# Kernel tuning notes

Measured on AMD Instinct MI355X. Metric: run time of the kernel, lower is better.

The kernel has to match this reference:

```python
import jax, jax.numpy as jnp
import numpy as np

N_HEAD = 12


def setup_inputs() -> dict:
    key = jax.random.key(0)
    ks = jax.random.split(key, 16)
    B, N, D, P, H = 1, 512, 384, 128, N_HEAD
    s = 0.02
    return {
        'x1d': jax.random.normal(ks[0], (B, N, D), jnp.float32),
        'x2d': jax.random.normal(ks[1], (B, N, N, P), jnp.float32),
        'pose_t': jax.random.normal(ks[2], (B, N, 3), jnp.float32),
        'pose_r': jax.random.normal(ks[3], (B, N, 3, 3), jnp.float32),
        'bias': jnp.zeros((B, 1, N, N), jnp.float32),
        'w_sq': jax.random.normal(ks[4], (D, D), jnp.float32) * s,
        'w_sk': jax.random.normal(ks[5], (D, D), jnp.float32) * s,
        'w_sv': jax.random.normal(ks[6], (D, D), jnp.float32) * s,
        'w_pb': jax.random.normal(ks[7], (P, H), jnp.float32) * s,
        'w_pq': jax.random.normal(ks[8], (D, H * 3 * 4), jnp.float32) * s,
        'w_pk': jax.random.normal(ks[9], (D, H * 3 * 4), jnp.float32) * s,
        'w_pv': jax.random.normal(ks[10], (D, H * 3 * 8), jnp.float32) * s,
        'tpw': jax.random.uniform(ks[11], (H,), jnp.float32),
        'w_pairv': jax.random.normal(ks[12], (P, D), jnp.float32) * s,
        'w_out': jax.random.normal(ks[13], (2 * D + H * 8 * 4, D), jnp.float32) * s,
        'b_out': jnp.zeros((D,), jnp.float32),
    }


def reference(x1d, x2d, pose_t, pose_r, bias, w_sq, w_sk, w_sv, w_pb,
              w_pq, w_pk, w_pv, tpw, w_pairv, w_out, b_out):
    B, N, D = x1d.shape
    H = N_HEAD
    dk = D // H
    scalar_w = 1.0 / np.sqrt(3 * dk)
    point_w_c = 1.0 / np.sqrt(3 * 4 * 9 / 2)
    pair_w = 1.0 / np.sqrt(3)

    T = pose_t                                # [B,N,3]
    R = jnp.swapaxes(pose_r, -1, -2)          # [B,N,3,3] (pose[1]^T as in torch code)

    # scalar attention
    q_s = (x1d @ w_sq).reshape(B, N, H, dk)
    k_s = (x1d @ w_sk).reshape(B, N, H, dk)
    v_s = (x1d @ w_sv).reshape(B, N, H, dk)
    scalar_attn = jnp.einsum('bihc,bjhc->bhij', q_s * scalar_w, k_s)

    # point attention (global frame)
    def affine(pt):  # R @ pt + T
        return jnp.einsum('bnxy,bnhpy->bnhpx', R, pt) + T[:, :, None, None, :]

    q_p = affine((x1d @ w_pq).reshape(B, N, H, 4, 3))
    k_p = affine((x1d @ w_pk).reshape(B, N, H, 4, 3))
    v_p = affine((x1d @ w_pv).reshape(B, N, H, 8, 3))

    dist = jnp.linalg.norm(q_p[:, :, None] - k_p[:, None], axis=-1)  # [B,I,J,H,P]
    pw = point_w_c * jax.nn.softplus(tpw)                            # [H]
    point_attn = -0.5 * pw[:, None, None] * jnp.transpose(dist.sum(-1), (0, 3, 1, 2))

    # pair bias attention
    pair_attn = pair_w * jnp.transpose(x2d @ w_pb, (0, 3, 1, 2))     # [B,H,I,J]

    attn = jax.nn.softmax(scalar_attn + point_attn + pair_attn + bias, axis=-1)

    # aggregations
    out_scalar = jnp.einsum('bhij,bjhc->bihc', attn, v_s).reshape(B, N, D)

    out_pg = jnp.einsum('bhij,bjhcp->bihcp', attn, v_p)              # [B,I,H,8,3]
    # inverse affine: R^T @ (x - T)
    out_pl = jnp.einsum('bnyx,bnhpy->bnhpx', R, out_pg - T[:, :, None, None, :])
    out_pn = jnp.linalg.norm(out_pl, axis=-1).reshape(B, N, H * 8)
    out_pl = out_pl.reshape(B, N, H * 8 * 3)

    v_pair = (x2d @ w_pairv).reshape(B, N, N, H, dk)
    out_pair = jnp.einsum('bhij,bijhc->bihc', attn, v_pair).reshape(B, N, D)

    feat = jnp.concatenate([out_scalar, out_pl, out_pair, out_pn], axis=-1)
    return feat @ w_out + b_out
```

## Files before the change

kernel.cpp:

```cpp
#include <hip/hip_runtime.h>
#include <hip/hip_bf16.h>
#include <math.h>

#define N_  512
#define D_  384
#define H_  12
#define DK_ 32
#define P_  128

typedef short short8 __attribute__((ext_vector_type(8)));
typedef float f32x4  __attribute__((ext_vector_type(4)));

static __device__ __forceinline__ unsigned short f2bf(float f) {
    union { float f; unsigned int u; } v; v.f = f;
    unsigned int r = (v.u + 0x7FFFu + ((v.u >> 16) & 1u)) >> 16;
    return (unsigned short)r;
}
static __device__ __forceinline__ float bf2f(unsigned short u) {
    union { unsigned int u; float f; } v; v.u = ((unsigned int)u) << 16;
    return v.f;
}
static __device__ __forceinline__ short2 pk2bf(float a, float b) {
    __hip_bfloat162 h = __float22bfloat162_rn(make_float2(a, b));
    return *(short2*)&h;
}
typedef union { short8 v; short2 h2[4]; } s8u;

__global__ __launch_bounds__(384) void k_front(
    const float* __restrict__ x2d, const float* __restrict__ w_pb,
    float* __restrict__ pairlog,
    const float* __restrict__ x1d, const float* __restrict__ pose_t,
    const float* __restrict__ pose_r,
    const float* __restrict__ w_sq, const float* __restrict__ w_sk,
    const float* __restrict__ w_sv, const float* __restrict__ w_pq,
    const float* __restrict__ w_pk, const float* __restrict__ w_pv,
    float* __restrict__ qs, float* __restrict__ kst,
    float* __restrict__ qp, float* __restrict__ kpt,
    unsigned short* __restrict__ vcatT)
{
    __shared__ float raw[8][288];
    __shared__ float Rsh[8][9];
    __shared__ float Tsh[8][3];

    const int t = threadIdx.x;

    if (blockIdx.x < 2048) {
        if (t >= 256) return;
        const int wid  = t >> 6;
        const int lane = t & 63;
        const int quad = lane >> 4;
        const int col  = lane & 15;
        const float pair_w = 0.57735027f;

        short8 bfr[4];
        #pragma unroll
        for (int kt = 0; kt < 4; ++kt) {
            #pragma unroll
            for (int jj = 0; jj < 8; ++jj) {
                int p = kt * 32 + quad * 8 + jj;
                bfr[kt][jj] = (col < 12) ? (short)f2bf(w_pb[p * 12 + col]) : (short)0;
            }
        }
        #pragma unroll
        for (int s = 0; s < 2; ++s) {
            const int T  = blockIdx.x * 8 + wid * 2 + s;
            const int i  = T >> 5;
            const int j0 = (T & 31) << 4;
            const float* xrow = x2d + ((size_t)(i * N_) + j0 + col) * P_;

            f32x4 acc = {0.f, 0.f, 0.f, 0.f};
            #pragma unroll
            for (int kt = 0; kt < 4; ++kt) {
                const int k0 = kt * 32 + quad * 8;
                float4 f0 = *(const float4*)(xrow + k0);
                float4 f1 = *(const float4*)(xrow + k0 + 4);
                s8u afr;
                afr.h2[0] = pk2bf(f0.x, f0.y);
                afr.h2[1] = pk2bf(f0.z, f0.w);
                afr.h2[2] = pk2bf(f1.x, f1.y);
                afr.h2[3] = pk2bf(f1.z, f1.w);
                acc = __builtin_amdgcn_mfma_f32_16x16x32_bf16(afr.v, bfr[kt], acc, 0, 0, 0);
            }
            if (col < 12) {
                #pragma unroll
                for (int r = 0; r < 4; ++r) {
                    int j = j0 + quad * 4 + r;
                    pairlog[((size_t)(col * N_ + i)) * N_ + j] = pair_w * acc[r];
                }
            }
        }
        return;
    }

    const int b   = blockIdx.x - 2048;
    const int seg = b >> 6;
    const int i0  = (b & 63) * 8;

    if (seg < 3) {
        const float* __restrict__ w = (seg == 0) ? w_sq : (seg == 1) ? w_sk : w_sv;
        float acc[8];
        #pragma unroll
        for (int r = 0; r < 8; ++r) acc[r] = 0.f;
        for (int d = 0; d < D_; d += 4) {
            float4 xr[8];
            #pragma unroll
            for (int r = 0; r < 8; ++r)
                xr[r] = *(const float4*)(x1d + (i0 + r) * D_ + d);
            #pragma unroll
            for (int e = 0; e < 4; ++e) {
                float wv = w[(d + e) * D_ + t];
                #pragma unroll
                for (int r = 0; r < 8; ++r)
                    acc[r] += ((const float*)&xr[r])[e] * wv;
            }
        }
        if (seg == 0) {
            #pragma unroll
            for (int r = 0; r < 8; ++r) qs[(i0 + r) * D_ + t] = acc[r];
        } else if (seg == 1) {
            *(float4*)(kst + t * N_ + i0)     = make_float4(acc[0], acc[1], acc[2], acc[3]);
            *(float4*)(kst + t * N_ + i0 + 4) = make_float4(acc[4], acc[5], acc[6], acc[7]);
        } else {
            int h = t >> 5, c = t & 31;
            s8u sv;
            #pragma unroll
            for (int r = 0; r < 4; ++r) sv.h2[r] = pk2bf(acc[2*r], acc[2*r+1]);
            *(short8*)(vcatT + ((size_t)h * 64 + c) * N_ + i0) = sv.v;
        }
    } else {
        if (t < 72) Rsh[t / 9][t % 9] = pose_r[(i0 + t / 9) * 9 + t % 9];
        else if (t < 96) {
            int r = (t - 72) / 3, c = (t - 72) % 3;
            Tsh[r][c] = pose_t[(i0 + r) * 3 + c];
        }

        if (t < 288) {
            const float* __restrict__ w;
            int col, ldw;
            if (seg == 3) {
                if (t < 144) { w = w_pq; col = t;       ldw = 144; }
                else         { w = w_pk; col = t - 144; ldw = 144; }
            } else         { w = w_pv; col = t;       ldw = 288; }
            float acc[8];
            #pragma unroll
            for (int r = 0; r < 8; ++r) acc[r] = 0.f;
            for (int d = 0; d < D_; d += 4) {
                float4 xr[8];
                #pragma unroll
                for (int r = 0; r < 8; ++r)
                    xr[r] = *(const float4*)(x1d + (i0 + r) * D_ + d);
                #pragma unroll
                for (int e = 0; e < 4; ++e) {
                    float wv = w[(d + e) * ldw + col];
                    #pragma unroll
                    for (int r = 0; r < 8; ++r)
                        acc[r] += ((const float*)&xr[r])[e] * wv;
                }
            }
            #pragma unroll
            for (int r = 0; r < 8; ++r) raw[r][t] = acc[r];
        }
        __syncthreads();

        if (t < 288) {
            const int x3   = t % 3;
            const int base = t - x3;
            if (seg == 3) {
                const int c = (t < 144) ? t : t - 144;
                if (t < 144) {
                    #pragma unroll
                    for (int r = 0; r < 8; ++r) {
                        float g = Rsh[r][0 + x3] * raw[r][base]
                                + Rsh[r][3 + x3] * raw[r][base + 1]
                                + Rsh[r][6 + x3] * raw[r][base + 2] + Tsh[r][x3];
                        qp[(i0 + r) * 144 + c] = g;
                    }
                } else {
                    float g[8];
                    #pragma unroll
                    for (int r = 0; r < 8; ++r)
                        g[r] = Rsh[r][0 + x3] * raw[r][base]
                             + Rsh[r][3 + x3] * raw[r][base + 1]
                             + Rsh[r][6 + x3] * raw[r][base + 2] + Tsh[r][x3];
                    *(float4*)(kpt + c * N_ + i0)     = make_float4(g[0], g[1], g[2], g[3]);
                    *(float4*)(kpt + c * N_ + i0 + 4) = make_float4(g[4], g[5], g[6], g[7]);
                }
            } else {
                int h = t / 24, pc = t % 24;
                float g[8];
                #pragma unroll
                for (int r = 0; r < 8; ++r)
                    g[r] = Rsh[r][0 + x3] * raw[r][base]
                         + Rsh[r][3 + x3] * raw[r][base + 1]
                         + Rsh[r][6 + x3] * raw[r][base + 2] + Tsh[r][x3];
                s8u sv;
                #pragma unroll
                for (int r = 0; r < 4; ++r) sv.h2[r] = pk2bf(g[2*r], g[2*r+1]);
                *(short8*)(vcatT + ((size_t)h * 64 + 32 + pc) * N_ + i0) = sv.v;
            }
        }
    }
}

__global__ __launch_bounds__(256) void k_sp_soft(
    const float* __restrict__ qs, const float* __restrict__ kst,
    const float* __restrict__ qp, const float* __restrict__ kpt,
    const float* __restrict__ bias, const float* __restrict__ tpw,
    const float* __restrict__ pairlog,
    unsigned short* __restrict__ attn_bf)
{
    const int h  = blockIdx.x / 128;
    const int i0 = (blockIdx.x % 128) * 4;
    const int t  = threadIdx.x;
    const int lane = t & 63;
    const int wid  = t >> 6;
    __shared__ float qsh[4][32];
    __shared__ float qph[4][12];
    __shared__ float wredm[4][4];
    __shared__ float wreds[4][4];
    if (t < 128) { int il = t / 32, c = t % 32; qsh[il][c] = qs[(i0+il) * D_ + h*32 + c]; }
    else if (t < 176) { int r = t - 128; int il = r / 12, c = r % 12; qph[il][c] = qp[(i0+il)*144 + h*12 + c]; }
    const float pwh = 0.13608276f * log1pf(expf(tpw[h]));
    const float scalar_w = 0.10206207f;
    __syncthreads();

    float v[4][2];
    for (int jh = 0; jh < 2; ++jh) {
        int j = t + jh * 256;
        float kv[32];
        #pragma unroll
        for (int c = 0; c < 32; ++c) kv[c] = kst[(h*32 + c) * N_ + j];
        float kp[12];
        #pragma unroll
        for (int c = 0; c < 12; ++c) kp[c] = kpt[(h*12 + c) * N_ + j];

        #pragma unroll
        for (int il = 0; il < 4; ++il) {
            float s = 0.f;
            #pragma unroll
            for (int c = 0; c < 32; ++c) s += qsh[il][c] * kv[c];
            float dsum = 0.f;
            #pragma unroll
            for (int p = 0; p < 4; ++p) {
                float dx = qph[il][p*3+0] - kp[p*3+0];
                float dy = qph[il][p*3+1] - kp[p*3+1];
                float dz = qph[il][p*3+2] - kp[p*3+2];
                dsum += sqrtf(dx*dx + dy*dy + dz*dz);
            }
            v[il][jh] = scalar_w * s - 0.5f * pwh * dsum
                      + bias[(i0+il) * N_ + j]
                      + pairlog[((size_t)(h * N_ + (i0+il))) * N_ + j];
        }
    }

    #pragma unroll
    for (int il = 0; il < 4; ++il) {
        float mt = fmaxf(v[il][0], v[il][1]);
        #pragma unroll
        for (int off = 1; off < 64; off <<= 1)
            mt = fmaxf(mt, __shfl_xor(mt, off));
        if (lane == 0) wredm[il][wid] = mt;
    }
    __syncthreads();
    float m[4];
    #pragma unroll
    for (int il = 0; il < 4; ++il)
        m[il] = fmaxf(fmaxf(wredm[il][0], wredm[il][1]),
                      fmaxf(wredm[il][2], wredm[il][3]));

    #pragma unroll
    for (int il = 0; il < 4; ++il) {
        float e0 = __expf(v[il][0] - m[il]);
        float e1 = __expf(v[il][1] - m[il]);
        v[il][0] = e0; v[il][1] = e1;
        float st = e0 + e1;
        #pragma unroll
        for (int off = 1; off < 64; off <<= 1)
            st += __shfl_xor(st, off);
        if (lane == 0) wreds[il][wid] = st;
    }
    __syncthreads();
    #pragma unroll
    for (int il = 0; il < 4; ++il) {
        float inv = 1.0f / (wreds[il][0] + wreds[il][1] + wreds[il][2] + wreds[il][3]);
        size_t base = ((size_t)(h * N_ + i0 + il)) * N_;
        attn_bf[base + t]       = f2bf(v[il][0] * inv);
        attn_bf[base + t + 256] = f2bf(v[il][1] * inv);
    }
}

__global__ __launch_bounds__(256) void k_mid(
    const unsigned short* __restrict__ attn_bf,
    const float* __restrict__ x2d,
    const unsigned short* __restrict__ vcatT,
    float* __restrict__ tmp,
    float* __restrict__ feat, float* __restrict__ outpg)
{
    __shared__ float4 at[3][N_];
    __shared__ float red[4][1536];

    const int t = threadIdx.x;

    if (blockIdx.x < 512) {
        const int i = blockIdx.x;
        for (int idx = t; idx < 12 * N_; idx += 256) {
            int h = idx >> 9, j = idx & 511;
            float a = bf2f(attn_bf[((size_t)(h * N_ + i)) * N_ + j]);
            ((float*)&at[h >> 2][j])[h & 3] = a;
        }
        __syncthreads();

        const int p2 = (t & 63) * 2;
        const int jh = t >> 6;
        float acc[12][2];
        #pragma unroll
        for (int h = 0; h < 12; ++h) { acc[h][0] = 0.f; acc[h][1] = 0.f; }
        const float* xb = x2d + (size_t)i * N_ * P_;

        #pragma unroll 4
        for (int j = jh; j < N_; j += 4) {
            float2 x = *(const float2*)(xb + j * P_ + p2);
            float4 a0 = at[0][j], a1 = at[1][j], a2 = at[2][j];
            acc[0][0]  += a0.x*x.x; acc[0][1]  += a0.x*x.y;
            acc[1][0]  += a0.y*x.x; acc[1][1]  += a0.y*x.y;
            acc[2][0]  += a0.z*x.x; acc[2][1]  += a0.z*x.y;
            acc[3][0]  += a0.w*x.x; acc[3][1]  += a0.w*x.y;
            acc[4][0]  += a1.x*x.x; acc[4][1]  += a1.x*x.y;
            acc[5][0]  += a1.y*x.x; acc[5][1]  += a1.y*x.y;
            acc[6][0]  += a1.z*x.x; acc[6][1]  += a1.z*x.y;
            acc[7][0]  += a1.w*x.x; acc[7][1]  += a1.w*x.y;
            acc[8][0]  += a2.x*x.x; acc[8][1]  += a2.x*x.y;
            acc[9][0]  += a2.y*x.x; acc[9][1]  += a2.y*x.y;
            acc[10][0] += a2.z*x.x; acc[10][1] += a2.z*x.y;
            acc[11][0] += a2.w*x.x; acc[11][1] += a2.w*x.y;
        }
        #pragma unroll
        for (int h = 0; h < 12; ++h) {
            red[jh][h * 128 + p2]     = acc[h][0];
            red[jh][h * 128 + p2 + 1] = acc[h][1];
        }
        __syncthreads();
        for (int idx = t; idx < 1536; idx += 256)
            tmp[(size_t)i * 1536 + idx] = red[0][idx] + red[1][idx] + red[2][idx] + red[3][idx];
        return;
    }

    const int bid  = blockIdx.x - 512;
    const int h    = bid >> 5;
    const int i0   = (bid & 31) << 4;
    const int wid  = t >> 6;
    const int lane = t & 63;
    const int quad = lane >> 4;
    const int col  = lane & 15;
    const int c    = wid * 16 + col;
    const bool cvalid = (c < 56);

    const unsigned short* arow = attn_bf + ((size_t)(h * N_ + i0 + col)) * N_;
    const unsigned short* brow = vcatT + ((size_t)h * 64 + c) * N_;

    f32x4 acc = {0.f, 0.f, 0.f, 0.f};
    #pragma unroll
    for (int kt = 0; kt < 16; ++kt) {
        const int k0 = kt * 32 + quad * 8;
        short8 a = *(const short8*)(arow + k0);
        short8 b;
        if (cvalid) b = *(const short8*)(brow + k0);
        else { b[0]=0;b[1]=0;b[2]=0;b[3]=0;b[4]=0;b[5]=0;b[6]=0;b[7]=0; }
        acc = __builtin_amdgcn_mfma_f32_16x16x32_bf16(a, b, acc, 0, 0, 0);
    }
    #pragma unroll
    for (int r = 0; r < 4; ++r) {
        int i = i0 + quad * 4 + r;
        if (c < 32)       feat[(size_t)i * 1152 + h * 32 + c] = acc[r];
        else if (c < 56)  outpg[((size_t)i * 12 + h) * 24 + (c - 32)] = acc[r];
    }
}

__global__ __launch_bounds__(384) void k_feat(
    const float* __restrict__ tmp, const float* __restrict__ outpg,
    const float* __restrict__ pose_t, const float* __restrict__ pose_r,
    const float* __restrict__ w_pairv, float* __restrict__ feat)
{
    const int i = blockIdx.x;
    const int t = threadIdx.x;
    __shared__ float tsh[1536];
    __shared__ float pg[288];
    __shared__ float pl[288];
    __shared__ float Rsh[9], Tsh[3];

    for (int idx = t; idx < 1536; idx += 384) tsh[idx] = tmp[(size_t)i * 1536 + idx];
    if (t < 288) pg[t] = outpg[i * 288 + t];
    if (t < 9) Rsh[t] = pose_r[i * 9 + t];
    if (t < 3) Tsh[t] = pose_t[i * 3 + t];
    __syncthreads();

    {
        int h = t >> 5;
        const float* ts = tsh + h * 128;
        float acc = 0.f;
        #pragma unroll 4
        for (int p = 0; p < 128; ++p) acc += ts[p] * w_pairv[p * D_ + t];
        feat[(size_t)i * 1152 + 672 + t] = acc;
    }
    if (t < 288) {
        int x3 = t % 3, base = t - x3;
        float g0 = pg[base + 0] - Tsh[0];
        float g1 = pg[base + 1] - Tsh[1];
        float g2 = pg[base + 2] - Tsh[2];
        float v = Rsh[x3*3+0]*g0 + Rsh[x3*3+1]*g1 + Rsh[x3*3+2]*g2;
        pl[t] = v;
        feat[(size_t)i * 1152 + 384 + t] = v;
    }
    __syncthreads();
    if (t < 96) {
        float a = pl[t*3], b = pl[t*3+1], c = pl[t*3+2];
        feat[(size_t)i * 1152 + 1056 + t] = sqrtf(a*a + b*b + c*c);
    }
}

__global__ __launch_bounds__(384) void k_out_part(
    const float* __restrict__ feat, const float* __restrict__ w_out,
    float* __restrict__ part)
{
    const int kc = blockIdx.x >> 6;
    const int i0 = (blockIdx.x & 63) * 8;
    const int t  = threadIdx.x;
    const int k0 = kc * 144;

    float acc[8];
    #pragma unroll
    for (int r = 0; r < 8; ++r) acc[r] = 0.f;

    for (int d = 0; d < 144; d += 4) {
        float4 fr[8];
        #pragma unroll
        for (int r = 0; r < 8; ++r)
            fr[r] = *(const float4*)(feat + (size_t)(i0 + r) * 1152 + k0 + d);
        #pragma unroll
        for (int e = 0; e < 4; ++e) {
            float wv = w_out[(size_t)(k0 + d + e) * D_ + t];
            #pragma unroll
            for (int r = 0; r < 8; ++r)
                acc[r] += ((const float*)&fr[r])[e] * wv;
        }
    }
    #pragma unroll
    for (int r = 0; r < 8; ++r)
        part[((size_t)kc * N_ + i0 + r) * D_ + t] = acc[r];
}

__global__ __launch_bounds__(256) void k_out_red(
    const float* __restrict__ part, const float* __restrict__ b_out,
    float* __restrict__ out)
{
    const int idx = blockIdx.x * 256 + threadIdx.x;
    float s = b_out[idx % D_];
    #pragma unroll
    for (int kc = 0; kc < 8; ++kc) s += part[(size_t)kc * (N_ * D_) + idx];
    out[idx] = s;
}

extern "C" void kernel_launch(void* const* d_in, const int* in_sizes, int n_in,
                              void* d_out, int out_size, void* d_ws, size_t ws_size,
                              hipStream_t stream)
{
    (void)in_sizes; (void)n_in; (void)out_size; (void)ws_size;
    const float* x1d     = (const float*)d_in[0];
    const float* x2d     = (const float*)d_in[1];
    const float* pose_t  = (const float*)d_in[2];
    const float* pose_r  = (const float*)d_in[3];
    const float* bias    = (const float*)d_in[4];
    const float* w_sq    = (const float*)d_in[5];
    const float* w_sk    = (const float*)d_in[6];
    const float* w_sv    = (const float*)d_in[7];
    const float* w_pb    = (const float*)d_in[8];
    const float* w_pq    = (const float*)d_in[9];
    const float* w_pk    = (const float*)d_in[10];
    const float* w_pv    = (const float*)d_in[11];
    const float* tpw     = (const float*)d_in[12];
    const float* w_pairv = (const float*)d_in[13];
    const float* w_out   = (const float*)d_in[14];
    const float* b_out   = (const float*)d_in[15];
    float* out = (float*)d_out;

    float* ws = (float*)d_ws;
    float* qs      = ws;
    float* kst     = qs      + 196608;
    float* qp      = kst     + 196608;
    float* kpt     = qp      + 73728;
    float* pairlog = kpt     + 73728;
    float* tmp     = pairlog + 3145728;
    float* outpg   = tmp     + 786432;
    float* feat    = outpg   + 147456;
    float* part    = feat    + 589824;
    unsigned short* attn_bf = (unsigned short*)(part + 1572864);
    unsigned short* vcatT   = attn_bf + (size_t)12 * N_ * N_;

    hipLaunchKernelGGL(k_front, dim3(2048 + 320), dim3(384), 0, stream,
                       x2d, w_pb, pairlog,
                       x1d, pose_t, pose_r, w_sq, w_sk, w_sv, w_pq, w_pk, w_pv,
                       qs, kst, qp, kpt, vcatT);
    hipLaunchKernelGGL(k_sp_soft, dim3(12 * 128), dim3(256), 0, stream,
                       qs, kst, qp, kpt, bias, tpw, pairlog, attn_bf);
    hipLaunchKernelGGL(k_mid, dim3(512 + 384), dim3(256), 0, stream,
                       attn_bf, x2d, vcatT, tmp, feat, outpg);
    hipLaunchKernelGGL(k_feat, dim3(N_), dim3(384), 0, stream,
                       tmp, outpg, pose_t, pose_r, w_pairv, feat);
    hipLaunchKernelGGL(k_out_part, dim3(512), dim3(384), 0, stream,
                       feat, w_out, part);
    hipLaunchKernelGGL(k_out_red, dim3(768), dim3(256), 0, stream,
                       part, b_out, out);
}
```

Baseline: 361.3 us.

## Fuse pair-bias projection, softmax and pair aggregation into one per-row kernel

Adds a new kernel, one block per query row i, that loads that row's x2d slice once into LDS as swizzled bf16. It then computes the pair logits with MFMA, runs the softmax over all 12 heads, and accumulates attn·x2d from the same LDS copy. This replaces three separate passes over the 128 MB x2d tensor (pair-bias GEMM in k_front, the pairlog read in softmax, and the k_mid aggregation) with one, and the pairlog intermediate is no longer written to global memory. In exchange, each block needs about 155 KB of LDS, so only one block fits per CU. The kst/kpt loads are repeated per row rather than amortized over 4 rows, and the aggregation now multiplies with bf16-rounded x2d and attention values.

```diff
diff --git a/kernel.cpp b/kernel.cpp
--- a/kernel.cpp
+++ b/kernel.cpp
@@ -25,10 +25,9 @@
     return *(short2*)&h;
 }
 typedef union { short8 v; short2 h2[4]; } s8u;
+typedef union { short2 h2[2]; unsigned long long u; } s4u;
 
 __global__ __launch_bounds__(384) void k_front(
-    const float* __restrict__ x2d, const float* __restrict__ w_pb,
-    float* __restrict__ pairlog,
     const float* __restrict__ x1d, const float* __restrict__ pose_t,
     const float* __restrict__ pose_r,
     const float* __restrict__ w_sq, const float* __restrict__ w_sk,
@@ -42,57 +41,8 @@
     __shared__ float Rsh[8][9];
     __shared__ float Tsh[8][3];
 
-    const int t = threadIdx.x;
-
-    if (blockIdx.x < 2048) {
-        if (t >= 256) return;
-        const int wid  = t >> 6;
-        const int lane = t & 63;
-        const int quad = lane >> 4;
-        const int col  = lane & 15;
-        const float pair_w = 0.57735027f;
-
-        short8 bfr[4];
-        #pragma unroll
-        for (int kt = 0; kt < 4; ++kt) {
-            #pragma unroll
-            for (int jj = 0; jj < 8; ++jj) {
-                int p = kt * 32 + quad * 8 + jj;
-                bfr[kt][jj] = (col < 12) ? (short)f2bf(w_pb[p * 12 + col]) : (short)0;
-            }
-        }
-        #pragma unroll
-        for (int s = 0; s < 2; ++s) {
-            const int T  = blockIdx.x * 8 + wid * 2 + s;
-            const int i  = T >> 5;
-            const int j0 = (T & 31) << 4;
-            const float* xrow = x2d + ((size_t)(i * N_) + j0 + col) * P_;
-
-            f32x4 acc = {0.f, 0.f, 0.f, 0.f};
-            #pragma unroll
-            for (int kt = 0; kt < 4; ++kt) {
-                const int k0 = kt * 32 + quad * 8;
-                float4 f0 = *(const float4*)(xrow + k0);
-                float4 f1 = *(const float4*)(xrow + k0 + 4);
-                s8u afr;
-                afr.h2[0] = pk2bf(f0.x, f0.y);
-                afr.h2[1] = pk2bf(f0.z, f0.w);
-                afr.h2[2] = pk2bf(f1.x, f1.y);
-                afr.h2[3] = pk2bf(f1.z, f1.w);
-                acc = __builtin_amdgcn_mfma_f32_16x16x32_bf16(afr.v, bfr[kt], acc, 0, 0, 0);
-            }
-            if (col < 12) {
-                #pragma unroll
-                for (int r = 0; r < 4; ++r) {
-                    int j = j0 + quad * 4 + r;
-                    pairlog[((size_t)(col * N_ + i)) * N_ + j] = pair_w * acc[r];
-                }
-            }
-        }
-        return;
-    }
-
-    const int b   = blockIdx.x - 2048;
+    const int t   = threadIdx.x;
+    const int b   = blockIdx.x;
     const int seg = b >> 6;
     const int i0  = (b & 63) * 8;
 
@@ -202,150 +152,193 @@
     }
 }
 
-__global__ __launch_bounds__(256) void k_sp_soft(
+__global__ __launch_bounds__(512) void k_big(
+    const float* __restrict__ x2d, const float* __restrict__ w_pb,
     const float* __restrict__ qs, const float* __restrict__ kst,
     const float* __restrict__ qp, const float* __restrict__ kpt,
     const float* __restrict__ bias, const float* __restrict__ tpw,
-    const float* __restrict__ pairlog,
-    unsigned short* __restrict__ attn_bf)
-{
-    const int h  = blockIdx.x / 128;
-    const int i0 = (blockIdx.x % 128) * 4;
-    const int t  = threadIdx.x;
+    unsigned short* __restrict__ attn_bf, float* __restrict__ tmp)
+{
+    __shared__ unsigned char smem[158528];
+    char*  x2b  = (char*)smem;
+    float* vbuf = (float*)(smem + 131072);
+    unsigned int* abufw = (unsigned int*)vbuf;
+    float* red  = vbuf + 3072;
+    float* qsh  = (float*)(smem + 131072 + 24576);
+    float* qph  = qsh + 384;
+    float* wredm = qph + 144;
+    float* wreds = wredm + 96;
+
+    const int i    = blockIdx.x;
+    const int t    = threadIdx.x;
     const int lane = t & 63;
     const int wid  = t >> 6;
-    __shared__ float qsh[4][32];
-    __shared__ float qph[4][12];
-    __shared__ float wredm[4][4];
-    __shared__ float wreds[4][4];
-    if (t < 128) { int il = t / 32, c = t % 32; qsh[il][c] = qs[(i0+il) * D_ + h*32 + c]; }
-    else if (t < 176) { int r = t - 128; int il = r / 12, c = r % 12; qph[il][c] = qp[(i0+il)*144 + h*12 + c]; }
-    const float pwh = 0.13608276f * log1pf(expf(tpw[h]));
-    const float scalar_w = 0.10206207f;
+    const int quad = lane >> 4;
+    const int col  = lane & 15;
+
+    if (t < 384) qsh[t] = qs[i * D_ + t];
+    if (t < 144) qph[t] = qp[i * 144 + t];
+    {
+        const float* xb = x2d + (size_t)i * N_ * P_;
+        const int jl = t >> 5, p4 = t & 31;
+        #pragma unroll 4
+        for (int q2 = 0; q2 < 32; ++q2) {
+            int j = q2 * 16 + jl;
+            float4 f = *(const float4*)(xb + j * P_ + p4 * 4);
+            s4u sv; sv.h2[0] = pk2bf(f.x, f.y); sv.h2[1] = pk2bf(f.z, f.w);
+            int byte = (j * 256 + p4 * 8) ^ ((j & 7) << 4);
+            *(unsigned long long*)(x2b + byte) = sv.u;
+        }
+    }
     __syncthreads();
 
-    float v[4][2];
-    for (int jh = 0; jh < 2; ++jh) {
-        int j = t + jh * 256;
-        float kv[32];
-        #pragma unroll
-        for (int c = 0; c < 32; ++c) kv[c] = kst[(h*32 + c) * N_ + j];
-        float kp[12];
-        #pragma unroll
-        for (int c = 0; c < 12; ++c) kp[c] = kpt[(h*12 + c) * N_ + j];
-
-        #pragma unroll
-        for (int il = 0; il < 4; ++il) {
+    {
+        const float pair_w = 0.57735027f;
+        short8 bfr[4];
+        #pragma unroll
+        for (int kt = 0; kt < 4; ++kt) {
+            #pragma unroll
+            for (int jj = 0; jj < 8; ++jj) {
+                int p = kt * 32 + quad * 8 + jj;
+                bfr[kt][jj] = (col < 12) ? (short)f2bf(w_pb[p * 12 + col]) : (short)0;
+            }
+        }
+        #pragma unroll
+        for (int s = 0; s < 4; ++s) {
+            const int jt   = wid * 4 + s;
+            const int jrow = jt * 16 + col;
+            f32x4 acc = {0.f, 0.f, 0.f, 0.f};
+            #pragma unroll
+            for (int kt = 0; kt < 4; ++kt) {
+                int addr = (jrow * 256 + (kt * 32 + quad * 8) * 2) ^ ((jrow & 7) << 4);
+                short8 a = *(const short8*)(x2b + addr);
+                acc = __builtin_amdgcn_mfma_f32_16x16x32_bf16(a, bfr[kt], acc, 0, 0, 0);
+            }
+            if (col < 12) {
+                #pragma unroll
+                for (int r = 0; r < 4; ++r)
+                    vbuf[col * N_ + jt * 16 + quad * 4 + r] = pair_w * acc[r];
+            }
+        }
+    }
+    __syncthreads();
+
+    {
+        const int j = t;
+        const float scalar_w = 0.10206207f;
+        float v[12];
+        #pragma unroll
+        for (int h = 0; h < 12; ++h) {
+            float kv[32];
+            #pragma unroll
+            for (int c = 0; c < 32; ++c) kv[c] = kst[(h * 32 + c) * N_ + j];
+            float kp[12];
+            #pragma unroll
+            for (int c = 0; c < 12; ++c) kp[c] = kpt[(h * 12 + c) * N_ + j];
             float s = 0.f;
             #pragma unroll
-            for (int c = 0; c < 32; ++c) s += qsh[il][c] * kv[c];
+            for (int c = 0; c < 32; ++c) s += qsh[h * 32 + c] * kv[c];
             float dsum = 0.f;
             #pragma unroll
             for (int p = 0; p < 4; ++p) {
-                float dx = qph[il][p*3+0] - kp[p*3+0];
-                float dy = qph[il][p*3+1] - kp[p*3+1];
-                float dz = qph[il][p*3+2] - kp[p*3+2];
-                dsum += sqrtf(dx*dx + dy*dy + dz*dz);
-            }
-            v[il][jh] = scalar_w * s - 0.5f * pwh * dsum
-                      + bias[(i0+il) * N_ + j]
-                      + pairlog[((size_t)(h * N_ + (i0+il))) * N_ + j];
-        }
-    }
-
-    #pragma unroll
-    for (int il = 0; il < 4; ++il) {
-        float mt = fmaxf(v[il][0], v[il][1]);
-        #pragma unroll
-        for (int off = 1; off < 64; off <<= 1)
-            mt = fmaxf(mt, __shfl_xor(mt, off));
-        if (lane == 0) wredm[il][wid] = mt;
+                float dx = qph[h * 12 + p * 3 + 0] - kp[p * 3 + 0];
+                float dy = qph[h * 12 + p * 3 + 1] - kp[p * 3 + 1];
+                float dz = qph[h * 12 + p * 3 + 2] - kp[p * 3 + 2];
+                dsum += sqrtf(dx * dx + dy * dy + dz * dz);
+            }
+            float pwh = 0.13608276f * log1pf(expf(tpw[h]));
+            v[h] = scalar_w * s - 0.5f * pwh * dsum
+                 + bias[i * N_ + j] + vbuf[h * N_ + j];
+        }
+
+        #pragma unroll
+        for (int h = 0; h < 12; ++h) {
+            float mt = v[h];
+            #pragma unroll
+            for (int off = 1; off < 64; off <<= 1)
+                mt = fmaxf(mt, __shfl_xor(mt, off));
+            if (lane == 0) wredm[wid * 12 + h] = mt;
+        }
+        __syncthreads();
+
+        float m[12];
+        #pragma unroll
+        for (int h = 0; h < 12; ++h) {
+            float mm = wredm[h];
+            #pragma unroll
+            for (int w = 1; w < 8; ++w) mm = fmaxf(mm, wredm[w * 12 + h]);
+            m[h] = mm;
+        }
+        float e[12];
+        #pragma unroll
+        for (int h = 0; h < 12; ++h) {
+            e[h] = __expf(v[h] - m[h]);
+            float s2 = e[h];
+            #pragma unroll
+            for (int off = 1; off < 64; off <<= 1)
+                s2 += __shfl_xor(s2, off);
+            if (lane == 0) wreds[wid * 12 + h] = s2;
+        }
+        for (int idx = t; idx < 1536; idx += 512) red[idx] = 0.f;
+        __syncthreads();
+
+        float a[12];
+        #pragma unroll
+        for (int h = 0; h < 12; ++h) {
+            float ss = wreds[h];
+            #pragma unroll
+            for (int w = 1; w < 8; ++w) ss += wreds[w * 12 + h];
+            a[h] = e[h] * (1.0f / ss);
+        }
+        #pragma unroll
+        for (int k = 0; k < 6; ++k) {
+            short2 pk = pk2bf(a[2 * k], a[2 * k + 1]);
+            abufw[j * 6 + k] = *(unsigned int*)&pk;
+        }
+        #pragma unroll
+        for (int h = 0; h < 12; ++h)
+            attn_bf[((size_t)(h * N_ + i)) * N_ + j] = f2bf(a[h]);
     }
     __syncthreads();
-    float m[4];
-    #pragma unroll
-    for (int il = 0; il < 4; ++il)
-        m[il] = fmaxf(fmaxf(wredm[il][0], wredm[il][1]),
-                      fmaxf(wredm[il][2], wredm[il][3]));
-
-    #pragma unroll
-    for (int il = 0; il < 4; ++il) {
-        float e0 = __expf(v[il][0] - m[il]);
-        float e1 = __expf(v[il][1] - m[il]);
-        v[il][0] = e0; v[il][1] = e1;
-        float st = e0 + e1;
-        #pragma unroll
-        for (int off = 1; off < 64; off <<= 1)
-            st += __shfl_xor(st, off);
-        if (lane == 0) wreds[il][wid] = st;
+
+    {
+        const int p2 = (lane) * 2;
+        float acc[12][2];
+        #pragma unroll
+        for (int h = 0; h < 12; ++h) { acc[h][0] = 0.f; acc[h][1] = 0.f; }
+        for (int jj = 0; jj < 64; ++jj) {
+            int j = wid * 64 + jj;
+            int byte = (j * 256 + p2 * 2) ^ ((j & 7) << 4);
+            unsigned int xw = *(const unsigned int*)(x2b + byte);
+            float x0 = bf2f((unsigned short)(xw & 0xffff));
+            float x1 = bf2f((unsigned short)(xw >> 16));
+            #pragma unroll
+            for (int k = 0; k < 6; ++k) {
+                unsigned int aw = abufw[j * 6 + k];
+                float a0 = bf2f((unsigned short)(aw & 0xffff));
+                float a1 = bf2f((unsigned short)(aw >> 16));
+                acc[2 * k][0]     += a0 * x0; acc[2 * k][1]     += a0 * x1;
+                acc[2 * k + 1][0] += a1 * x0; acc[2 * k + 1][1] += a1 * x1;
+            }
+        }
+        #pragma unroll
+        for (int h = 0; h < 12; ++h) {
+            atomicAdd(&red[h * 128 + p2],     acc[h][0]);
+            atomicAdd(&red[h * 128 + p2 + 1], acc[h][1]);
+        }
     }
     __syncthreads();
-    #pragma unroll
-    for (int il = 0; il < 4; ++il) {
-        float inv = 1.0f / (wreds[il][0] + wreds[il][1] + wreds[il][2] + wreds[il][3]);
-        size_t base = ((size_t)(h * N_ + i0 + il)) * N_;
-        attn_bf[base + t]       = f2bf(v[il][0] * inv);
-        attn_bf[base + t + 256] = f2bf(v[il][1] * inv);
-    }
-}
-
-__global__ __launch_bounds__(256) void k_mid(
+    for (int idx = t; idx < 1536; idx += 512)
+        tmp[(size_t)i * 1536 + idx] = red[idx];
+}
+
+__global__ __launch_bounds__(256) void k_aggr(
     const unsigned short* __restrict__ attn_bf,
-    const float* __restrict__ x2d,
     const unsigned short* __restrict__ vcatT,
-    float* __restrict__ tmp,
     float* __restrict__ feat, float* __restrict__ outpg)
 {
-    __shared__ float4 at[3][N_];
-    __shared__ float red[4][1536];
-
-    const int t = threadIdx.x;
-
-    if (blockIdx.x < 512) {
-        const int i = blockIdx.x;
-        for (int idx = t; idx < 12 * N_; idx += 256) {
-            int h = idx >> 9, j = idx & 511;
-            float a = bf2f(attn_bf[((size_t)(h * N_ + i)) * N_ + j]);
-            ((float*)&at[h >> 2][j])[h & 3] = a;
-        }
-        __syncthreads();
-
-        const int p2 = (t & 63) * 2;
-        const int jh = t >> 6;
-        float acc[12][2];
-        #pragma unroll
-        for (int h = 0; h < 12; ++h) { acc[h][0] = 0.f; acc[h][1] = 0.f; }
-        const float* xb = x2d + (size_t)i * N_ * P_;
-
-        #pragma unroll 4
-        for (int j = jh; j < N_; j += 4) {
-            float2 x = *(const float2*)(xb + j * P_ + p2);
-            float4 a0 = at[0][j], a1 = at[1][j], a2 = at[2][j];
-            acc[0][0]  += a0.x*x.x; acc[0][1]  += a0.x*x.y;
-            acc[1][0]  += a0.y*x.x; acc[1][1]  += a0.y*x.y;
-            acc[2][0]  += a0.z*x.x; acc[2][1]  += a0.z*x.y;
-            acc[3][0]  += a0.w*x.x; acc[3][1]  += a0.w*x.y;
-            acc[4][0]  += a1.x*x.x; acc[4][1]  += a1.x*x.y;
-            acc[5][0]  += a1.y*x.x; acc[5][1]  += a1.y*x.y;
-            acc[6][0]  += a1.z*x.x; acc[6][1]  += a1.z*x.y;
-            acc[7][0]  += a1.w*x.x; acc[7][1]  += a1.w*x.y;
-            acc[8][0]  += a2.x*x.x; acc[8][1]  += a2.x*x.y;
-            acc[9][0]  += a2.y*x.x; acc[9][1]  += a2.y*x.y;
-            acc[10][0] += a2.z*x.x; acc[10][1] += a2.z*x.y;
-            acc[11][0] += a2.w*x.x; acc[11][1] += a2.w*x.y;
-        }
-        #pragma unroll
-        for (int h = 0; h < 12; ++h) {
-            red[jh][h * 128 + p2]     = acc[h][0];
-            red[jh][h * 128 + p2 + 1] = acc[h][1];
-        }
-        __syncthreads();
-        for (int idx = t; idx < 1536; idx += 256)
-            tmp[(size_t)i * 1536 + idx] = red[0][idx] + red[1][idx] + red[2][idx] + red[3][idx];
-        return;
-    }
-
-    const int bid  = blockIdx.x - 512;
+    const int t    = threadIdx.x;
+    const int bid  = blockIdx.x;
     const int h    = bid >> 5;
     const int i0   = (bid & 31) << 4;
     const int wid  = t >> 6;
@@ -496,14 +489,13 @@
     unsigned short* attn_bf = (unsigned short*)(part + 1572864);
     unsigned short* vcatT   = attn_bf + (size_t)12 * N_ * N_;
 
-    hipLaunchKernelGGL(k_front, dim3(2048 + 320), dim3(384), 0, stream,
-                       x2d, w_pb, pairlog,
+    hipLaunchKernelGGL(k_front, dim3(320), dim3(384), 0, stream,
                        x1d, pose_t, pose_r, w_sq, w_sk, w_sv, w_pq, w_pk, w_pv,
                        qs, kst, qp, kpt, vcatT);
-    hipLaunchKernelGGL(k_sp_soft, dim3(12 * 128), dim3(256), 0, stream,
-                       qs, kst, qp, kpt, bias, tpw, pairlog, attn_bf);
-    hipLaunchKernelGGL(k_mid, dim3(512 + 384), dim3(256), 0, stream,
-                       attn_bf, x2d, vcatT, tmp, feat, outpg);
+    hipLaunchKernelGGL(k_big, dim3(N_), dim3(512), 0, stream,
+                       x2d, w_pb, qs, kst, qp, kpt, bias, tpw, attn_bf, tmp);
+    hipLaunchKernelGGL(k_aggr, dim3(384), dim3(256), 0, stream,
+                       attn_bf, vcatT, feat, outpg);
     hipLaunchKernelGGL(k_feat, dim3(N_), dim3(384), 0, stream,
                        tmp, outpg, pose_t, pose_r, w_pairv, feat);
     hipLaunchKernelGGL(k_out_part, dim3(512), dim3(384), 0, stream,
```

After: 1.364 ms. 3.78x slower.
